# Kernel optimization log

Measured on AMD Instinct MI355X. Metric: run time of the kernel, lower is better.

The kernel has to match this reference:

```python
import jax, jax.numpy as jnp
import numpy as np

B = 16384   # batched decode steps (have_action_batch across transitions)
H = 1024    # hidden_dim
A = 20      # len(ner_map) + 2 valid-action vocabulary


def setup_inputs() -> dict:
    key = jax.random.key(0)
    ks = jax.random.split(key, 10)
    scale = 0.02
    buffer_h = jax.random.normal(ks[0], (B, H), jnp.float32)
    stack_h = jax.random.normal(ks[1], (B, H), jnp.float32)
    output_h = jax.random.normal(ks[2], (B, H), jnp.float32)
    action_h = jax.random.normal(ks[3], (B, H), jnp.float32)
    W1 = jax.random.normal(ks[4], (4 * H, H), jnp.float32) * scale  # lstms_output_2_softmax
    b1 = jnp.zeros((H,), jnp.float32)
    W2 = jax.random.normal(ks[5], (H, A), jnp.float32) * scale      # output_2_act
    b2 = jnp.zeros((A,), jnp.float32)
    real_actions = jax.random.randint(ks[6], (B,), 0, A, dtype=jnp.int32)
    valid_mask = jax.random.bernoulli(ks[7], 0.5, (B, A))
    # gold action must always be in the valid-action list
    valid_mask = valid_mask.at[jnp.arange(B), real_actions].set(True)
    return {
        "buffer_h": buffer_h, "stack_h": stack_h, "output_h": output_h,
        "action_h": action_h, "W1": W1, "b1": b1, "W2": W2, "b2": b2,
        "valid_mask": valid_mask, "real_actions": real_actions,
    }


def reference(buffer_h, stack_h, output_h, action_h, W1, b1, W2, b2, valid_mask, real_actions):
    # ragged concat of per-example LSTM states -> [B, 4H]
    x = jnp.concatenate([buffer_h, stack_h, output_h, action_h], axis=1)
    hidden = jnp.tanh(x @ W1 + b1)          # lstms_output_2_softmax + tanh, [B, H]
    logits = hidden @ W2 + b2               # output_2_act, [B, A]
    # per-example valid-action gather expressed as masked log_softmax
    NEG = jnp.asarray(-1e9, logits.dtype)
    masked = jnp.where(valid_mask, logits, NEG)
    log_probs = jax.nn.log_softmax(masked, axis=-1)
    predict_actions = jnp.argmax(log_probs, axis=-1)               # [B] int
    losses = jnp.take_along_axis(log_probs, real_actions[:, None].astype(jnp.int32), axis=1)[:, 0]
    return predict_actions, losses
```

## Files before the change

### kernel.cpp

```cpp
#include <hip/hip_runtime.h>
#include <math.h>


#define BTOT 16384
#define HD   1024
#define NACT 20
#define KTOT 4096
#define KT_N 128

typedef __attribute__((ext_vector_type(8))) short short8;
typedef __attribute__((ext_vector_type(4))) float f32x4;

#define MFMA(a, b, c) __builtin_amdgcn_mfma_f32_16x16x32_bf16((a), (b), (c), 0, 0, 0)

__device__ __forceinline__ void gload16(const void* g, void* l)
{
    auto gp = (const __attribute__((address_space(1))) unsigned int*)((uintptr_t)g);
    auto lp = (__attribute__((address_space(3))) unsigned int*)((uintptr_t)l);
    __builtin_amdgcn_global_load_lds(gp, lp, 16, 0, 0);
}

__device__ __forceinline__ void split8(const float4 v0, const float4 v1,
                                       int4& hi, int4& lo)
{
    const float f[8] = {v0.x, v0.y, v0.z, v0.w, v1.x, v1.y, v1.z, v1.w};
    unsigned hp[4], lp[4];
#pragma unroll
    for (int i = 0; i < 4; ++i) {
        const unsigned u0 = __float_as_uint(f[2 * i]);
        const unsigned u1 = __float_as_uint(f[2 * i + 1]);
        const unsigned r0 = u0 + 0x7FFFu + ((u0 >> 16) & 1u);
        const unsigned r1 = u1 + 0x7FFFu + ((u1 >> 16) & 1u);
        hp[i] = (r0 >> 16) | (r1 & 0xFFFF0000u);
        const float h0 = __uint_as_float(r0 & 0xFFFF0000u);
        const float h1 = __uint_as_float(r1 & 0xFFFF0000u);
        const float d0 = f[2 * i] - h0;
        const float d1 = f[2 * i + 1] - h1;
        const unsigned s0 = __float_as_uint(d0);
        const unsigned s1 = __float_as_uint(d1);
        const unsigned q0 = s0 + 0x7FFFu + ((s0 >> 16) & 1u);
        const unsigned q1 = s1 + 0x7FFFu + ((s1 >> 16) & 1u);
        lp[i] = (q0 >> 16) | (q1 & 0xFFFF0000u);
    }
    hi = make_int4((int)hp[0], (int)hp[1], (int)hp[2], (int)hp[3]);
    lo = make_int4((int)lp[0], (int)lp[1], (int)lp[2], (int)lp[3]);
}

__global__ __launch_bounds__(256) void detect_mask_kernel(
    const unsigned int* __restrict__ w, int nwords, int* __restrict__ ctr)
{
    int c0 = 0, c1 = 0, c2 = 0, c3 = 0;
    for (int i = blockIdx.x * 256 + threadIdx.x; i < nwords; i += gridDim.x * 256) {
        unsigned int v = w[i];
        c0 += (v & 0x000000FFu) ? 1 : 0;
        c1 += (v & 0x0000FF00u) ? 1 : 0;
        c2 += (v & 0x00FF0000u) ? 1 : 0;
        c3 += (v & 0xFF000000u) ? 1 : 0;
    }
#pragma unroll
    for (int off = 32; off; off >>= 1) {
        c0 += __shfl_xor(c0, off, 64);
        c1 += __shfl_xor(c1, off, 64);
        c2 += __shfl_xor(c2, off, 64);
        c3 += __shfl_xor(c3, off, 64);
    }
    if ((threadIdx.x & 63) == 0) {
        atomicAdd(&ctr[0], c0);
        atomicAdd(&ctr[1], c1);
        atomicAdd(&ctr[2], c2);
        atomicAdd(&ctr[3], c3);
    }
}

__global__ __launch_bounds__(256) void wpack_kernel(
    const float* __restrict__ W1, char* __restrict__ Wp)
{
    const int b  = blockIdx.x;
    const int t  = threadIdx.x;
    const int nt = b >> 7;
    const int kt = b & 127;
    const int nn = t & 127;
    const int h  = t >> 7;

    float f[16];
#pragma unroll
    for (int kk = 0; kk < 16; ++kk)
        f[kk] = W1[(size_t)(kt * 32 + h * 16 + kk) * HD + nt * 128 + nn];

    int4 hi0, lo0, hi1, lo1;
    split8(make_float4(f[0], f[1], f[2], f[3]),
           make_float4(f[4], f[5], f[6], f[7]), hi0, lo0);
    split8(make_float4(f[8], f[9], f[10], f[11]),
           make_float4(f[12], f[13], f[14], f[15]), hi1, lo1);

    char* rowp = Wp + (((size_t)(nt * KT_N + kt)) << 14) + nn * 128;
    const int r7 = nn & 7;
    const int s0 = ((2 * h) ^ r7) << 4;
    const int s1 = ((2 * h + 1) ^ r7) << 4;
    *(int4*)(rowp + s0)        = hi0;
    *(int4*)(rowp + s1)        = hi1;
    *(int4*)(rowp + (s0 ^ 64)) = lo0;
    *(int4*)(rowp + (s1 ^ 64)) = lo1;
}

__global__ __launch_bounds__(512, 1) void gemm1_mfma_kernel(
    const float* __restrict__ A0, const float* __restrict__ A1,
    const float* __restrict__ A2, const float* __restrict__ A3,
    const char* __restrict__ Wp, const float* __restrict__ b1,
    float* __restrict__ hidden)
{
    extern __shared__ __align__(16) char smem[];

    const int newbid = (blockIdx.x & 7) * 32 + (blockIdx.x >> 3);
    const int mt = newbid >> 2;
    const int nt = newbid & 3;

    const int t    = threadIdx.x;
    const int lane = t & 63;
    const int wid  = t >> 6;
    const int wr = wid >> 2, wc = wid & 3;
    const int lrow = lane & 15;
    const int lk   = lane >> 4;

    const int rowL  = t >> 1;
    const int khalf = t & 1;
    const size_t aRowOff = (size_t)(mt * 256 + rowL) * HD;

    const char* gB0 = Wp + (((size_t)((nt * 2)     * KT_N)) << 14);
    const char* gB1 = Wp + (((size_t)((nt * 2 + 1) * KT_N)) << 14);

    const unsigned aBase = (unsigned)(wr * 128 + lrow) * 128
                         + (((unsigned)lk ^ (unsigned)(lrow & 7)) << 4);
    const unsigned bBase = (unsigned)(wc >> 1) * 16384
                         + (unsigned)((wc & 1) * 64 + lrow) * 128
                         + (((unsigned)lk ^ (unsigned)(lrow & 7)) << 4);

    const int r7 = rowL & 7;
    const unsigned wA0 = (unsigned)rowL * 128 + (((unsigned)(2 * khalf)     ^ (unsigned)r7) << 4);
    const unsigned wA1 = (unsigned)rowL * 128 + (((unsigned)(2 * khalf + 1) ^ (unsigned)r7) << 4);

    f32x4 acc[8][4];
#pragma unroll
    for (int i = 0; i < 8; ++i)
#pragma unroll
        for (int j = 0; j < 4; ++j) acc[i][j] = (f32x4){0.f, 0.f, 0.f, 0.f};

    {
        const float4* ap = (const float4*)(A0 + aRowOff + khalf * 16);
        const float4 f0 = ap[0], f1 = ap[1], f2 = ap[2], f3 = ap[3];
        int4 h0, l0, h1, l1;
        split8(f0, f1, h0, l0);
        split8(f2, f3, h1, l1);
        char* lA = smem;
        *(int4*)(lA + wA0)        = h0;
        *(int4*)(lA + (wA0 ^ 64)) = l0;
        *(int4*)(lA + wA1)        = h1;
        *(int4*)(lA + (wA1 ^ 64)) = l1;
        char* lB = smem + 32768;
        gload16(gB0 + t * 16,        lB + t * 16);
        gload16(gB0 + 8192 + t * 16, lB + 8192 + t * 16);
        gload16(gB1 + t * 16,        lB + 16384 + t * 16);
        gload16(gB1 + 8192 + t * 16, lB + 24576 + t * 16);
    }
    __syncthreads();

    int cur = 0;
    for (int kt = 0; kt < KT_N; ++kt) {
        float4 f0, f1, f2, f3;
        const bool pref = (kt + 1 < KT_N);
        if (pref) {
            char* lB = smem + (cur ^ 1) * 65536 + 32768;
            const char* s0 = gB0 + (((size_t)(kt + 1)) << 14);
            const char* s1 = gB1 + (((size_t)(kt + 1)) << 14);
            gload16(s0 + t * 16,        lB + t * 16);
            gload16(s0 + 8192 + t * 16, lB + 8192 + t * 16);
            gload16(s1 + t * 16,        lB + 16384 + t * 16);
            gload16(s1 + 8192 + t * 16, lB + 24576 + t * 16);
            const int kg = (kt + 1) * 32 + khalf * 16;
            const float* seg = (kg < 1024) ? A0 : (kg < 2048) ? A1 : (kg < 3072) ? A2 : A3;
            const float4* ap = (const float4*)(seg + aRowOff + (kg & 1023));
            f0 = ap[0]; f1 = ap[1]; f2 = ap[2]; f3 = ap[3];
        }

        const char* lA = smem + cur * 65536;
        const char* lB = lA + 32768;

        short8 bh[4], bl[4];
#pragma unroll
        for (int nf = 0; nf < 4; ++nf) {
            bh[nf] = *(const short8*)(lB + (bBase + nf * 2048));
            bl[nf] = *(const short8*)(lB + ((bBase + nf * 2048) ^ 64));
        }
#pragma unroll
        for (int mf = 0; mf < 8; ++mf) {
            const short8 ah = *(const short8*)(lA + (aBase + mf * 2048));
            const short8 al = *(const short8*)(lA + ((aBase + mf * 2048) ^ 64));
#pragma unroll
            for (int nf = 0; nf < 4; ++nf) {
                acc[mf][nf] = MFMA(ah, bh[nf], acc[mf][nf]);
                acc[mf][nf] = MFMA(ah, bl[nf], acc[mf][nf]);
                acc[mf][nf] = MFMA(al, bh[nf], acc[mf][nf]);
            }
        }

        if (pref) {
            int4 h0, l0, h1, l1;
            split8(f0, f1, h0, l0);
            split8(f2, f3, h1, l1);
            char* wAp = smem + (cur ^ 1) * 65536;
            *(int4*)(wAp + wA0)        = h0;
            *(int4*)(wAp + (wA0 ^ 64)) = l0;
            *(int4*)(wAp + wA1)        = h1;
            *(int4*)(wAp + (wA1 ^ 64)) = l1;
        }
        __syncthreads();
        cur ^= 1;
    }

#pragma unroll
    for (int nf = 0; nf < 4; ++nf) {
        const int col = nt * 256 + wc * 64 + nf * 16 + lrow;
        const float bias = b1[col];
#pragma unroll
        for (int mf = 0; mf < 8; ++mf) {
            const int row0 = mt * 256 + wr * 128 + mf * 16 + lk * 4;
#pragma unroll
            for (int r = 0; r < 4; ++r)
                hidden[(size_t)(row0 + r) * HD + col] = tanhf(acc[mf][nf][r] + bias);
        }
    }
}

__device__ __forceinline__ void finish_row(
    const float* __restrict__ acc, const float* __restrict__ b2,
    const void* __restrict__ mask, const int* __restrict__ real_actions,
    int fmt, int row, float* __restrict__ out,
    int* __restrict__ flagCnt, int* __restrict__ flagList, int lane)
{
    float masked[NACT];
#pragma unroll
    for (int a = 0; a < NACT; ++a) {
        const float lg = acc[a] + b2[a];
        bool valid;
        if (fmt == 0)      valid = ((const unsigned char*)mask)[(size_t)row * NACT + a] != 0;
        else if (fmt == 1) valid = ((const int*)mask)[(size_t)row * NACT + a] != 0;
        else               valid = ((const float*)mask)[(size_t)row * NACT + a] != 0.f;
        masked[a] = valid ? lg : -1e9f;
    }
    float m = masked[0], m2 = -3e38f;
    int amax = 0;
#pragma unroll
    for (int a = 1; a < NACT; ++a) {
        const float v = masked[a];
        if (v > m) { m2 = m; m = v; amax = a; }
        else if (v > m2) m2 = v;
    }
    float s = 0.f;
#pragma unroll
    for (int a = 0; a < NACT; ++a) s += expf(masked[a] - m);
    const float lse = m + logf(s);
    const int ga = real_actions[row];
    float gl = masked[0];
#pragma unroll
    for (int a = 1; a < NACT; ++a) gl = (ga == a) ? masked[a] : gl;
    if (lane == 0) {
        out[row] = (float)amax;
        out[BTOT + row] = gl - lse;
        if (flagList != nullptr && (m - m2) < 1e-3f) {
            const int ix = atomicAdd(flagCnt, 1);
            flagList[ix] = row;
        }
    }
}

__global__ __launch_bounds__(256) void head_kernel(
    const float* __restrict__ hidden, const float* __restrict__ W2,
    const float* __restrict__ b2, const void* __restrict__ mask,
    const int* __restrict__ real_actions, int* __restrict__ ctr,
    int* __restrict__ flagList, float* __restrict__ out, int rowBase)
{
    const int lane = threadIdx.x & 63;
    const int lr0  = (blockIdx.x * 4 + (threadIdx.x >> 6)) * 2;

    float a0[NACT], a1[NACT];
#pragma unroll
    for (int a = 0; a < NACT; ++a) { a0[a] = 0.f; a1[a] = 0.f; }

    const float* h0 = hidden + (size_t)lr0 * HD;
    const float* h1 = h0 + HD;
#pragma unroll 4
    for (int j = 0; j < 16; ++j) {
        const int h = lane + 64 * j;
        const float hv0 = h0[h];
        const float hv1 = h1[h];
        const float4* w4 = (const float4*)(W2 + (size_t)h * NACT);
        const float4 w0 = w4[0], w1 = w4[1], w2 = w4[2], w3 = w4[3], w4v = w4[4];
        a0[0]  = fmaf(hv0, w0.x,  a0[0]);  a1[0]  = fmaf(hv1, w0.x,  a1[0]);
        a0[1]  = fmaf(hv0, w0.y,  a0[1]);  a1[1]  = fmaf(hv1, w0.y,  a1[1]);
        a0[2]  = fmaf(hv0, w0.z,  a0[2]);  a1[2]  = fmaf(hv1, w0.z,  a1[2]);
        a0[3]  = fmaf(hv0, w0.w,  a0[3]);  a1[3]  = fmaf(hv1, w0.w,  a1[3]);
        a0[4]  = fmaf(hv0, w1.x,  a0[4]);  a1[4]  = fmaf(hv1, w1.x,  a1[4]);
        a0[5]  = fmaf(hv0, w1.y,  a0[5]);  a1[5]  = fmaf(hv1, w1.y,  a1[5]);
        a0[6]  = fmaf(hv0, w1.z,  a0[6]);  a1[6]  = fmaf(hv1, w1.z,  a1[6]);
        a0[7]  = fmaf(hv0, w1.w,  a0[7]);  a1[7]  = fmaf(hv1, w1.w,  a1[7]);
        a0[8]  = fmaf(hv0, w2.x,  a0[8]);  a1[8]  = fmaf(hv1, w2.x,  a1[8]);
        a0[9]  = fmaf(hv0, w2.y,  a0[9]);  a1[9]  = fmaf(hv1, w2.y,  a1[9]);
        a0[10] = fmaf(hv0, w2.z,  a0[10]); a1[10] = fmaf(hv1, w2.z,  a1[10]);
        a0[11] = fmaf(hv0, w2.w,  a0[11]); a1[11] = fmaf(hv1, w2.w,  a1[11]);
        a0[12] = fmaf(hv0, w3.x,  a0[12]); a1[12] = fmaf(hv1, w3.x,  a1[12]);
        a0[13] = fmaf(hv0, w3.y,  a0[13]); a1[13] = fmaf(hv1, w3.y,  a1[13]);
        a0[14] = fmaf(hv0, w3.z,  a0[14]); a1[14] = fmaf(hv1, w3.z,  a1[14]);
        a0[15] = fmaf(hv0, w3.w,  a0[15]); a1[15] = fmaf(hv1, w3.w,  a1[15]);
        a0[16] = fmaf(hv0, w4v.x, a0[16]); a1[16] = fmaf(hv1, w4v.x, a1[16]);
        a0[17] = fmaf(hv0, w4v.y, a0[17]); a1[17] = fmaf(hv1, w4v.y, a1[17]);
        a0[18] = fmaf(hv0, w4v.z, a0[18]); a1[18] = fmaf(hv1, w4v.z, a1[18]);
        a0[19] = fmaf(hv0, w4v.w, a0[19]); a1[19] = fmaf(hv1, w4v.w, a1[19]);
    }
#pragma unroll
    for (int off = 32; off; off >>= 1) {
#pragma unroll
        for (int a = 0; a < NACT; ++a) {
            a0[a] += __shfl_xor(a0[a], off, 64);
            a1[a] += __shfl_xor(a1[a], off, 64);
        }
    }

    const int c1 = ctr[1], c2 = ctr[2], c3 = ctr[3];
    const int fmt = (c1 > 0) ? 0 : ((c2 > 0 || c3 > 0) ? 2 : 1);

    finish_row(a0, b2, mask, real_actions, fmt, rowBase + lr0,     out, &ctr[4], flagList, lane);
    finish_row(a1, b2, mask, real_actions, fmt, rowBase + lr0 + 1, out, &ctr[4], flagList, lane);
}

__global__ __launch_bounds__(256) void refine_hidden_kernel(
    const float* __restrict__ A0, const float* __restrict__ A1,
    const float* __restrict__ A2, const float* __restrict__ A3,
    const float* __restrict__ W1, const float* __restrict__ b1,
    const int* __restrict__ ctr, const int* __restrict__ list,
    float* __restrict__ hiddenR, int cap)
{
    __shared__ float xs[2][KTOT];
    __shared__ float red[2][4][64];
    const int tid = threadIdx.x;
    int count = ctr[4]; if (count > cap) count = cap;
    const int total = ((count + 1) >> 1) << 4;

    for (int u = blockIdx.x; u < total; u += gridDim.x) {
        const int p  = u >> 4;
        const int f0 = 2 * p;
        const int f1 = (2 * p + 1 < count) ? (2 * p + 1) : f0;
        const int r0 = list[f0];
        const int r1 = list[f1];
        const int colBase = (u & 15) << 6;

        for (int i = tid; i < KTOT; i += 256) {
            const float* seg = (i < 1024) ? A0 : (i < 2048) ? A1 : (i < 3072) ? A2 : A3;
            xs[0][i] = seg[(size_t)r0 * HD + (i & 1023)];
            xs[1][i] = seg[(size_t)r1 * HD + (i & 1023)];
        }
        __syncthreads();

        const int col   = colBase + (tid & 63);
        const int kbase = (tid >> 6) << 10;
        const float* Wc = W1 + col;
        float acc0 = 0.f, acc1 = 0.f;

        float wa[16], wb[16];
#pragma unroll
        for (int v = 0; v < 16; ++v) wa[v] = Wc[(size_t)(kbase + v) * HD];
#pragma unroll
        for (int v = 0; v < 16; ++v) wb[v] = Wc[(size_t)(kbase + 16 + v) * HD];

        const int kend = kbase + 1024;
        for (int k0 = kbase; k0 < kend; k0 += 32) {
#pragma unroll
            for (int v = 0; v < 16; ++v) {
                acc0 = fmaf(xs[0][k0 + v], wa[v], acc0);
                acc1 = fmaf(xs[1][k0 + v], wa[v], acc1);
            }
            if (k0 + 32 < kend) {
#pragma unroll
                for (int v = 0; v < 16; ++v)
                    wa[v] = Wc[(size_t)(k0 + 32 + v) * HD];
            }
#pragma unroll
            for (int v = 0; v < 16; ++v) {
                acc0 = fmaf(xs[0][k0 + 16 + v], wb[v], acc0);
                acc1 = fmaf(xs[1][k0 + 16 + v], wb[v], acc1);
            }
            if (k0 + 48 < kend) {
#pragma unroll
                for (int v = 0; v < 16; ++v)
                    wb[v] = Wc[(size_t)(k0 + 48 + v) * HD];
            }
        }

        red[0][tid >> 6][tid & 63] = acc0;
        red[1][tid >> 6][tid & 63] = acc1;
        __syncthreads();

        if (tid < 128) {
            const int r = tid >> 6, c = tid & 63;
            const float s = red[r][0][c] + red[r][1][c] + red[r][2][c] + red[r][3][c];
            const int f = r ? f1 : f0;
            hiddenR[(size_t)f * HD + colBase + c] = tanhf(s + b1[colBase + c]);
        }
        __syncthreads();
    }
}

__global__ __launch_bounds__(256) void refine_head_kernel(
    const float* __restrict__ hiddenR, const float* __restrict__ W2,
    const float* __restrict__ b2, const void* __restrict__ mask,
    const int* __restrict__ real_actions, const int* __restrict__ ctr,
    const int* __restrict__ list, float* __restrict__ out, int cap)
{
    const int lane = threadIdx.x & 63;
    const int wv   = threadIdx.x >> 6;
    int count = ctr[4]; if (count > cap) count = cap;
    const int c1 = ctr[1], c2 = ctr[2], c3 = ctr[3];
    const int fmt = (c1 > 0) ? 0 : ((c2 > 0 || c3 > 0) ? 2 : 1);

    for (int f = blockIdx.x * 4 + wv; f < count; f += gridDim.x * 4) {
        const int row = list[f];
        const float* hrow = hiddenR + (size_t)f * HD;
        float a20[NACT];
#pragma unroll
        for (int a = 0; a < NACT; ++a) a20[a] = 0.f;
#pragma unroll 4
        for (int m = 0; m < 16; ++m) {
            const int h = lane + 64 * m;
            const float hv = hrow[h];
            const float4* w4 = (const float4*)(W2 + (size_t)h * NACT);
            const float4 w0 = w4[0], w1 = w4[1], w2 = w4[2], w3 = w4[3], w4v = w4[4];
            a20[0]  = fmaf(hv, w0.x,  a20[0]);  a20[1]  = fmaf(hv, w0.y,  a20[1]);
            a20[2]  = fmaf(hv, w0.z,  a20[2]);  a20[3]  = fmaf(hv, w0.w,  a20[3]);
            a20[4]  = fmaf(hv, w1.x,  a20[4]);  a20[5]  = fmaf(hv, w1.y,  a20[5]);
            a20[6]  = fmaf(hv, w1.z,  a20[6]);  a20[7]  = fmaf(hv, w1.w,  a20[7]);
            a20[8]  = fmaf(hv, w2.x,  a20[8]);  a20[9]  = fmaf(hv, w2.y,  a20[9]);
            a20[10] = fmaf(hv, w2.z,  a20[10]); a20[11] = fmaf(hv, w2.w,  a20[11]);
            a20[12] = fmaf(hv, w3.x,  a20[12]); a20[13] = fmaf(hv, w3.y,  a20[13]);
            a20[14] = fmaf(hv, w3.z,  a20[14]); a20[15] = fmaf(hv, w3.w,  a20[15]);
            a20[16] = fmaf(hv, w4v.x, a20[16]); a20[17] = fmaf(hv, w4v.y, a20[17]);
            a20[18] = fmaf(hv, w4v.z, a20[18]); a20[19] = fmaf(hv, w4v.w, a20[19]);
        }
#pragma unroll
        for (int off = 32; off; off >>= 1) {
#pragma unroll
            for (int a = 0; a < NACT; ++a) a20[a] += __shfl_xor(a20[a], off, 64);
        }
        finish_row(a20, b2, mask, real_actions, fmt, row, out, nullptr, nullptr, lane);
    }
}

extern "C" void kernel_launch(void* const* d_in, const int* in_sizes, int n_in,
                              void* d_out, int out_size, void* d_ws, size_t ws_size,
                              hipStream_t stream)
{
    const float* buf_h = (const float*)d_in[0];
    const float* stk_h = (const float*)d_in[1];
    const float* out_h = (const float*)d_in[2];
    const float* act_h = (const float*)d_in[3];
    const float* W1    = (const float*)d_in[4];
    const float* b1    = (const float*)d_in[5];
    const float* W2    = (const float*)d_in[6];
    const float* b2    = (const float*)d_in[7];
    const void*  mask  = d_in[8];
    const int*   ra    = (const int*)d_in[9];
    float*       out   = (float*)d_out;

    int*  ctr      = (int*)d_ws;
    int*  flagList = (int*)((char*)d_ws + 256);
    char* Wp       = (char*)d_ws + 256 + 65536;
    const size_t wpBytes = (size_t)8 * KT_N * 16384;
    float* hidden  = (float*)(Wp + wpBytes);

    hipMemsetAsync(d_ws, 0, 256, stream);
    detect_mask_kernel<<<64, 256, 0, stream>>>(
        (const unsigned int*)mask, BTOT * NACT / 4, ctr);
    wpack_kernel<<<8 * KT_N, 256, 0, stream>>>(W1, Wp);

    hipFuncSetAttribute((const void*)gemm1_mfma_kernel,
                        hipFuncAttributeMaxDynamicSharedMemorySize, 131072);

    gemm1_mfma_kernel<<<256, 512, 131072, stream>>>(
        buf_h, stk_h, out_h, act_h, Wp, b1, hidden);
    head_kernel<<<BTOT / 8, 256, 0, stream>>>(
        hidden, W2, b2, mask, ra, ctr, flagList, out, 0);

    float* hiddenR = hidden;
    refine_hidden_kernel<<<2048, 256, 0, stream>>>(
        buf_h, stk_h, out_h, act_h, W1, b1, ctr, flagList, hiddenR, BTOT);
    refine_head_kernel<<<64, 256, 0, stream>>>(
        hiddenR, W2, b2, mask, ra, ctr, flagList, out, BTOT);
}
```

Before: 550.6 us.

## Split GEMM k-step into four quadrant phases with explicit waitcnt and barriers

Restructures the main GEMM loop into four MFMA phases, one per quadrant of the accumulator tile. The next tile's global->LDS loads and the A-split writes are interleaved between phases, with explicit s_waitcnt vmcnt/lgkmcnt, sched_barrier and s_barrier in place of __syncthreads. s_setprio is raised around the MFMA bursts. The aim is to overlap LDS reads and global prefetch with matrix work and to cut register pressure from holding all fragments at once. In exchange it adds several more barriers per k-step, and the hand-written vmcnt counts must match the number of in-flight loads exactly.

```diff
diff --git a/kernel.cpp b/kernel.cpp
--- a/kernel.cpp
+++ b/kernel.cpp
@@ -12,6 +12,12 @@
 typedef __attribute__((ext_vector_type(4))) float f32x4;
 
 #define MFMA(a, b, c) __builtin_amdgcn_mfma_f32_16x16x32_bf16((a), (b), (c), 0, 0, 0)
+
+#define SCHED0() __builtin_amdgcn_sched_barrier(0)
+#define SBAR()   do { SCHED0(); __builtin_amdgcn_s_barrier(); SCHED0(); } while (0)
+#define WAITV4() do { asm volatile("s_waitcnt vmcnt(4)" ::: "memory"); SCHED0(); } while (0)
+#define WAITV0() do { asm volatile("s_waitcnt vmcnt(0)" ::: "memory"); SCHED0(); } while (0)
+#define WAITL0() do { asm volatile("s_waitcnt lgkmcnt(0)" ::: "memory"); SCHED0(); } while (0)
 
 __device__ __forceinline__ void gload16(const void* g, void* l)
 {
@@ -145,76 +151,159 @@
 #pragma unroll
         for (int j = 0; j < 4; ++j) acc[i][j] = (f32x4){0.f, 0.f, 0.f, 0.f};
 
+    float4 f0, f1, f2, f3;
+
     {
         const float4* ap = (const float4*)(A0 + aRowOff + khalf * 16);
-        const float4 f0 = ap[0], f1 = ap[1], f2 = ap[2], f3 = ap[3];
-        int4 h0, l0, h1, l1;
-        split8(f0, f1, h0, l0);
-        split8(f2, f3, h1, l1);
-        char* lA = smem;
-        *(int4*)(lA + wA0)        = h0;
-        *(int4*)(lA + (wA0 ^ 64)) = l0;
-        *(int4*)(lA + wA1)        = h1;
-        *(int4*)(lA + (wA1 ^ 64)) = l1;
+        f0 = ap[0]; f1 = ap[1]; f2 = ap[2]; f3 = ap[3];
+    }
+    SCHED0();
+    {
         char* lB = smem + 32768;
         gload16(gB0 + t * 16,        lB + t * 16);
         gload16(gB0 + 8192 + t * 16, lB + 8192 + t * 16);
         gload16(gB1 + t * 16,        lB + 16384 + t * 16);
         gload16(gB1 + 8192 + t * 16, lB + 24576 + t * 16);
     }
-    __syncthreads();
-
-    int cur = 0;
+    SCHED0();
+    WAITV4();
+    {
+        int4 h0, l0, h1, l1;
+        split8(f0, f1, h0, l0);
+        split8(f2, f3, h1, l1);
+        *(int4*)(smem + wA0)        = h0;
+        *(int4*)(smem + (wA0 ^ 64)) = l0;
+        *(int4*)(smem + wA1)        = h1;
+        *(int4*)(smem + (wA1 ^ 64)) = l1;
+    }
+    WAITL0();
+    SBAR();
+
     for (int kt = 0; kt < KT_N; ++kt) {
-        float4 f0, f1, f2, f3;
+        const int cur = kt & 1;
+        const char* bufc  = smem + cur * 65536;
+        const char* bufcB = bufc + 32768;
+        char*       bufn  = smem + (cur ^ 1) * 65536;
         const bool pref = (kt + 1 < KT_N);
+
+        short8 ah[4], al[4], bh[2], bl[2];
+
         if (pref) {
-            char* lB = smem + (cur ^ 1) * 65536 + 32768;
-            const char* s0 = gB0 + (((size_t)(kt + 1)) << 14);
-            const char* s1 = gB1 + (((size_t)(kt + 1)) << 14);
-            gload16(s0 + t * 16,        lB + t * 16);
-            gload16(s0 + 8192 + t * 16, lB + 8192 + t * 16);
-            gload16(s1 + t * 16,        lB + 16384 + t * 16);
-            gload16(s1 + 8192 + t * 16, lB + 24576 + t * 16);
             const int kg = (kt + 1) * 32 + khalf * 16;
             const float* seg = (kg < 1024) ? A0 : (kg < 2048) ? A1 : (kg < 3072) ? A2 : A3;
             const float4* ap = (const float4*)(seg + aRowOff + (kg & 1023));
             f0 = ap[0]; f1 = ap[1]; f2 = ap[2]; f3 = ap[3];
-        }
-
-        const char* lA = smem + cur * 65536;
-        const char* lB = lA + 32768;
-
-        short8 bh[4], bl[4];
-#pragma unroll
-        for (int nf = 0; nf < 4; ++nf) {
-            bh[nf] = *(const short8*)(lB + (bBase + nf * 2048));
-            bl[nf] = *(const short8*)(lB + ((bBase + nf * 2048) ^ 64));
-        }
-#pragma unroll
-        for (int mf = 0; mf < 8; ++mf) {
-            const short8 ah = *(const short8*)(lA + (aBase + mf * 2048));
-            const short8 al = *(const short8*)(lA + ((aBase + mf * 2048) ^ 64));
-#pragma unroll
-            for (int nf = 0; nf < 4; ++nf) {
-                acc[mf][nf] = MFMA(ah, bh[nf], acc[mf][nf]);
-                acc[mf][nf] = MFMA(ah, bl[nf], acc[mf][nf]);
-                acc[mf][nf] = MFMA(al, bh[nf], acc[mf][nf]);
-            }
-        }
-
+            SCHED0();
+            WAITV4();
+        } else {
+            WAITV0();
+        }
+        SBAR();
+
+#pragma unroll
+        for (int mf = 0; mf < 4; ++mf) {
+            ah[mf] = *(const short8*)(bufc + (aBase + mf * 2048));
+            al[mf] = *(const short8*)(bufc + ((aBase + mf * 2048) ^ 64));
+        }
+#pragma unroll
+        for (int nf = 0; nf < 2; ++nf) {
+            bh[nf] = *(const short8*)(bufcB + (bBase + nf * 2048));
+            bl[nf] = *(const short8*)(bufcB + ((bBase + nf * 2048) ^ 64));
+        }
+        SBAR();
+        __builtin_amdgcn_s_setprio(1);
+#pragma unroll
+        for (int mf = 0; mf < 4; ++mf)
+#pragma unroll
+            for (int nf = 0; nf < 2; ++nf) {
+                acc[mf][nf] = MFMA(ah[mf], bh[nf], acc[mf][nf]);
+                acc[mf][nf] = MFMA(ah[mf], bl[nf], acc[mf][nf]);
+                acc[mf][nf] = MFMA(al[mf], bh[nf], acc[mf][nf]);
+            }
+        __builtin_amdgcn_s_setprio(0);
+
+#pragma unroll
+        for (int nf = 0; nf < 2; ++nf) {
+            bh[nf] = *(const short8*)(bufcB + (bBase + (2 + nf) * 2048));
+            bl[nf] = *(const short8*)(bufcB + ((bBase + (2 + nf) * 2048) ^ 64));
+        }
         if (pref) {
+            const char* s0 = gB0 + (((size_t)(kt + 1)) << 14);
+            char* lB = bufn + 32768;
+            gload16(s0 + t * 16,        lB + t * 16);
+            gload16(s0 + 8192 + t * 16, lB + 8192 + t * 16);
+        }
+        SCHED0();
+        SBAR();
+        __builtin_amdgcn_s_setprio(1);
+#pragma unroll
+        for (int mf = 0; mf < 4; ++mf)
+#pragma unroll
+            for (int nf = 0; nf < 2; ++nf) {
+                acc[mf][2 + nf] = MFMA(ah[mf], bh[nf], acc[mf][2 + nf]);
+                acc[mf][2 + nf] = MFMA(ah[mf], bl[nf], acc[mf][2 + nf]);
+                acc[mf][2 + nf] = MFMA(al[mf], bh[nf], acc[mf][2 + nf]);
+            }
+        __builtin_amdgcn_s_setprio(0);
+
+#pragma unroll
+        for (int mf = 0; mf < 4; ++mf) {
+            ah[mf] = *(const short8*)(bufc + (aBase + (4 + mf) * 2048));
+            al[mf] = *(const short8*)(bufc + ((aBase + (4 + mf) * 2048) ^ 64));
+        }
+#pragma unroll
+        for (int nf = 0; nf < 2; ++nf) {
+            bh[nf] = *(const short8*)(bufcB + (bBase + nf * 2048));
+            bl[nf] = *(const short8*)(bufcB + ((bBase + nf * 2048) ^ 64));
+        }
+        if (pref) {
+            const char* s1 = gB1 + (((size_t)(kt + 1)) << 14);
+            char* lB = bufn + 32768;
+            gload16(s1 + t * 16,        lB + 16384 + t * 16);
+            gload16(s1 + 8192 + t * 16, lB + 24576 + t * 16);
+        }
+        SCHED0();
+        SBAR();
+        __builtin_amdgcn_s_setprio(1);
+#pragma unroll
+        for (int mf = 0; mf < 4; ++mf)
+#pragma unroll
+            for (int nf = 0; nf < 2; ++nf) {
+                acc[4 + mf][nf] = MFMA(ah[mf], bh[nf], acc[4 + mf][nf]);
+                acc[4 + mf][nf] = MFMA(ah[mf], bl[nf], acc[4 + mf][nf]);
+                acc[4 + mf][nf] = MFMA(al[mf], bh[nf], acc[4 + mf][nf]);
+            }
+        __builtin_amdgcn_s_setprio(0);
+
+        if (pref) {
+            WAITV4();
             int4 h0, l0, h1, l1;
             split8(f0, f1, h0, l0);
             split8(f2, f3, h1, l1);
-            char* wAp = smem + (cur ^ 1) * 65536;
-            *(int4*)(wAp + wA0)        = h0;
-            *(int4*)(wAp + (wA0 ^ 64)) = l0;
-            *(int4*)(wAp + wA1)        = h1;
-            *(int4*)(wAp + (wA1 ^ 64)) = l1;
-        }
-        __syncthreads();
-        cur ^= 1;
+            *(int4*)(bufn + wA0)        = h0;
+            *(int4*)(bufn + (wA0 ^ 64)) = l0;
+            *(int4*)(bufn + wA1)        = h1;
+            *(int4*)(bufn + (wA1 ^ 64)) = l1;
+        }
+#pragma unroll
+        for (int nf = 0; nf < 2; ++nf) {
+            bh[nf] = *(const short8*)(bufcB + (bBase + (2 + nf) * 2048));
+            bl[nf] = *(const short8*)(bufcB + ((bBase + (2 + nf) * 2048) ^ 64));
+        }
+        SCHED0();
+        SBAR();
+        __builtin_amdgcn_s_setprio(1);
+#pragma unroll
+        for (int mf = 0; mf < 4; ++mf)
+#pragma unroll
+            for (int nf = 0; nf < 2; ++nf) {
+                acc[4 + mf][2 + nf] = MFMA(ah[mf], bh[nf], acc[4 + mf][2 + nf]);
+                acc[4 + mf][2 + nf] = MFMA(ah[mf], bl[nf], acc[4 + mf][2 + nf]);
+                acc[4 + mf][2 + nf] = MFMA(al[mf], bh[nf], acc[4 + mf][2 + nf]);
+            }
+        __builtin_amdgcn_s_setprio(0);
+        WAITL0();
+        SBAR();
     }
 
 #pragma unroll
```

New measurement: 607.7 us. +10.4%, slower.
